# Kernel optimization log

Measured on AMD Instinct MI355X. Metric: run time of the kernel, lower is better.

The kernel has to match this reference:

```python
import jax, jax.numpy as jnp
import numpy as np

B, L = 128, 200
NUM_C, D, M = 10000, 128, 64


def setup_inputs() -> dict:
    key = jax.random.key(0)
    ks = jax.random.split(key, 16)
    n = lambda k, s, sc=0.05: jax.random.normal(k, s, dtype=jnp.float32) * sc
    return {
        "q": jax.random.randint(ks[0], (B, L), 0, NUM_C),
        "r": jax.random.randint(ks[1], (B, L), 0, 2),
        "k_emb": n(ks[2], (NUM_C, D)),
        "v_emb": n(ks[3], (2, D)),
        "Mk": n(ks[4], (M, D), 0.2),   # kaiming_normal_
        "Mv0": n(ks[5], (M, D), 0.2),  # kaiming_normal_
        "f_W": n(ks[6], (D, 2 * D)), "f_b": jnp.zeros((D,), jnp.float32),
        "e_W": n(ks[7], (D, D)), "e_b": jnp.zeros((D,), jnp.float32),
        "a_W": n(ks[8], (D, D)), "a_b": jnp.zeros((D,), jnp.float32),
        "ab_W": n(ks[9], (1, D)), "ab_b": jnp.zeros((1,), jnp.float32),
        "df_W": n(ks[10], (1, D)), "df_b": jnp.zeros((1,), jnp.float32),
    }


def reference(q, r, k_emb, v_emb, Mk, Mv0, f_W, f_b, e_W, e_b, a_W, a_b, ab_W, ab_b, df_W, df_b):
    # Embeddings
    k = k_emb[q]                # [B, L, D] question key embedding
    v = k + v_emb[r]            # [B, L, D] value embedding

    # Attention over memory slots, erase/add gates
    w = jax.nn.softmax(jnp.einsum('bld,md->blm', k, Mk), axis=-1)   # [B, L, M]
    e = jax.nn.sigmoid(jnp.einsum('bld,ed->ble', v, e_W) + e_b)      # erase [B, L, D]
    a = jnp.tanh(jnp.einsum('bld,ed->ble', v, a_W) + a_b)            # add   [B, L, D]

    Mvt0 = jnp.broadcast_to(Mv0[None], (q.shape[0], Mv0.shape[0], Mv0.shape[1]))  # [B, M, D]

    def step(Mvt, inp):
        wt, et, at = inp  # [B,M], [B,D], [B,D]
        # read uses memory BEFORE this timestep's write (Mv[:, :-1] in torch)
        read = jnp.einsum('bm,bmd->bd', wt, Mvt)
        we = wt[:, :, None]
        Mvt_new = Mvt * (1.0 - we * et[:, None, :]) + we * at[:, None, :]
        return Mvt_new, read

    _, reads = jax.lax.scan(
        step, Mvt0,
        (w.transpose(1, 0, 2), e.transpose(1, 0, 2), a.transpose(1, 0, 2)))
    reads = reads.transpose(1, 0, 2)  # [B, L, D]

    f = jnp.tanh(jnp.concatenate([reads, k], axis=-1) @ f_W.T + f_b)  # [B, L, D]
    stu_ability = jnp.tanh(f @ ab_W.T + ab_b)   # [B, L, 1] (dropout is identity in eval)
    que_diff = jnp.tanh(k @ df_W.T + df_b)      # [B, L, 1]
    p = jax.nn.sigmoid(3.0 * stu_ability - que_diff)
    return p.squeeze(-1)  # [B, L]
```

## Files before the change

kernel.cpp:

```cpp
#include <hip/hip_runtime.h>

typedef unsigned short ushort_t;
typedef _Float16 f16_t;
typedef short bf16x8 __attribute__((ext_vector_type(8)));
typedef float f32x4 __attribute__((ext_vector_type(4)));

#define B_ 128
#define L_ 200
#define D_ 128
#define M_ 64

__device__ __forceinline__ float fast_sigmoid(float x) {
    return 1.f / (1.f + __expf(-x));
}

__device__ __forceinline__ float fast_tanh(float x) {
    float xc = fminf(fmaxf(x, -15.f), 15.f);
    float e = __expf(2.f * xc);
    return (e - 1.f) / (e + 1.f);
}

__device__ __forceinline__ ushort_t f2bf(float f) {
    union { float f; unsigned int u; } x;
    x.f = f;
    unsigned int u = x.u;
    unsigned int r = (u + 0x7FFFu + ((u >> 16) & 1u)) >> 16;
    return (ushort_t)r;
}

__device__ __forceinline__ uint4 pack8(float4 a, float4 b) {
    uint4 u;
    u.x = (unsigned)f2bf(a.x) | ((unsigned)f2bf(a.y) << 16);
    u.y = (unsigned)f2bf(a.z) | ((unsigned)f2bf(a.w) << 16);
    u.z = (unsigned)f2bf(b.x) | ((unsigned)f2bf(b.y) << 16);
    u.w = (unsigned)f2bf(b.z) | ((unsigned)f2bf(b.w) << 16);
    return u;
}

__device__ __forceinline__ unsigned pack_ea(float e, float a) {
    union { f16_t h[2]; unsigned u; } p;
    p.h[0] = (f16_t)e;
    p.h[1] = (f16_t)a;
    return p.u;
}

__device__ __forceinline__ float2 unpack_ea(unsigned u) {
    union { unsigned u; f16_t h[2]; } p;
    p.u = u;
    float2 r;
    r.x = (float)p.h[0];
    r.y = (float)p.h[1];
    return r;
}

#define F_WQ   0u
#define F_EAQ  1638400u
#define F_FKQ  8192000u
#define F_RD   11468800u
#define F_DIFF 14745600u
#define F_PACK 14771200u
#define WPACK_N 57344
#define FPACK_N 16384

__global__ __launch_bounds__(256) void k_pack(
    const float* __restrict__ Mk, const float* __restrict__ eW,
    const float* __restrict__ aW, const float* __restrict__ fW,
    ushort_t* __restrict__ Wpack, ushort_t* __restrict__ Fpack)
{
    int i = blockIdx.x * 256 + threadIdx.x;
    if (i < WPACK_N) {
        int g = i >> 9, lane = (i >> 3) & 63, j = i & 7;
        int nt = g >> 2, ks = g & 3;
        int col = nt * 16 + (lane & 15);
        int d = ks * 32 + ((lane >> 4) << 3) + j;
        float v;
        if (col < 64)       v = Mk[col * 128 + d];
        else if (col < 192) v = eW[(col - 64) * 128 + d];
        else if (col < 320) v = aW[(col - 192) * 128 + d];
        else                v = fW[(col - 320) * 256 + 128 + d];
        Wpack[i] = f2bf(v);
    } else if (i < WPACK_N + FPACK_N) {
        int e = i - WPACK_N;
        int g = e >> 9, lane = (e >> 3) & 63, j = e & 7;
        int nt = g >> 2, ks = g & 3;
        int col = nt * 16 + (lane & 15);
        int d = ks * 32 + ((lane >> 4) << 3) + j;
        Fpack[e] = f2bf(fW[col * 256 + d]);
    }
}

__device__ __forceinline__ void loadB4(const ushort_t* __restrict__ base,
                                       int nt, int lane, bf16x8* b) {
    const ushort_t* p = base + (nt * 256 + lane) * 8;
    b[0] = *(const bf16x8*)(p);
    b[1] = *(const bf16x8*)(p + 512);
    b[2] = *(const bf16x8*)(p + 1024);
    b[3] = *(const bf16x8*)(p + 1536);
}

__global__ __launch_bounds__(512) void k_pre_mfma(
    const int* __restrict__ q, const int* __restrict__ r,
    const float* __restrict__ k_emb, const float* __restrict__ v_emb,
    const ushort_t* __restrict__ Wpack,
    const float* __restrict__ e_b, const float* __restrict__ a_b,
    const float* __restrict__ df_W, const float* __restrict__ df_b,
    float* __restrict__ wq, unsigned* __restrict__ eaq,
    f16_t* __restrict__ fkq, float* __restrict__ diffq)
{
    __shared__ ushort_t skA[8192];
    __shared__ ushort_t svA[8192];
    __shared__ float slog[64 * 68];

    const int tid = threadIdx.x;
    const int pos0 = blockIdx.x * 64;
    const int wave = tid >> 6;
    const int lane = tid & 63;
    const int mt = wave & 3;
    const int nh = wave >> 2;

    #pragma unroll
    for (int i = 0; i < 2; i++) {
        int E = tid + 512 * i;
        int mtile = E >> 8, ks = (E >> 6) & 3, le = E & 63;
        int prow = pos0 + mtile * 16 + (le & 15);
        int dof = ks * 32 + ((le >> 4) << 3);
        int qv = q[prow], rv = r[prow];
        const float4* kp = (const float4*)(k_emb + qv * 128 + dof);
        float4 ka = kp[0], kb = kp[1];
        const float4* vp = (const float4*)(v_emb + rv * 128 + dof);
        float4 va = vp[0], vb = vp[1];
        *(uint4*)&skA[E * 8] = pack8(ka, kb);
        float4 s0, s1;
        s0.x = ka.x + va.x; s0.y = ka.y + va.y; s0.z = ka.z + va.z; s0.w = ka.w + va.w;
        s1.x = kb.x + vb.x; s1.y = kb.y + vb.y; s1.z = kb.z + vb.z; s1.w = kb.w + vb.w;
        *(uint4*)&svA[E * 8] = pack8(s0, s1);
    }
    __syncthreads();

    bf16x8 A[4];
    {
        const ushort_t* src = nh ? svA : skA;
        #pragma unroll
        for (int ks = 0; ks < 4; ks++)
            A[ks] = *(const bf16x8*)&src[((mt * 4 + ks) * 64 + lane) * 8];
    }

    const int col = lane & 15;
    const int quad = lane >> 4;
    const int rbase = mt * 16 + quad * 4;

    if (nh == 0) {
        bf16x8 Bb[2][4];
        loadB4(Wpack, 0, lane, Bb[0]);
        #pragma unroll
        for (int j = 0; j < 12; j++) {
            if (j < 11) {
                int jn = j + 1;
                loadB4(Wpack, (jn < 4) ? jn : jn + 16, lane, Bb[jn & 1]);
            }
            f32x4 acc = {0.f, 0.f, 0.f, 0.f};
            #pragma unroll
            for (int ks = 0; ks < 4; ks++)
                acc = __builtin_amdgcn_mfma_f32_16x16x32_bf16(A[ks], Bb[j & 1][ks], acc, 0, 0, 0);
            if (j < 4) {
                #pragma unroll
                for (int reg = 0; reg < 4; reg++)
                    slog[(rbase + reg) * 68 + j * 16 + col] = acc[reg];
            } else {
                int c = (j - 4) * 16 + col;
                #pragma unroll
                for (int reg = 0; reg < 4; reg++)
                    fkq[(pos0 + rbase + reg) * 128 + c] = (f16_t)acc[reg];
            }
        }
        {
            int row = tid >> 2, ln = tid & 3;
            const float* lr = slog + row * 68 + ln * 16;
            float v[16];
            #pragma unroll
            for (int j = 0; j < 16; j++) v[j] = lr[j];
            float mx = v[0];
            #pragma unroll
            for (int j = 1; j < 16; j++) mx = fmaxf(mx, v[j]);
            mx = fmaxf(mx, __shfl_xor(mx, 1));
            mx = fmaxf(mx, __shfl_xor(mx, 2));
            float s = 0.f;
            #pragma unroll
            for (int j = 0; j < 16; j++) { v[j] = __expf(v[j] - mx); s += v[j]; }
            s += __shfl_xor(s, 1); s += __shfl_xor(s, 2);
            float inv = 1.f / s;
            float* wout = wq + (pos0 + row) * 64 + ln * 16;
            #pragma unroll
            for (int j4 = 0; j4 < 4; j4++) {
                float4 o;
                o.x = v[j4 * 4 + 0] * inv;
                o.y = v[j4 * 4 + 1] * inv;
                o.z = v[j4 * 4 + 2] * inv;
                o.w = v[j4 * 4 + 3] * inv;
                *(float4*)(wout + j4 * 4) = o;
            }
        }
    } else {
        bf16x8 Be[2][4], Ba[2][4];
        loadB4(Wpack, 4, lane, Be[0]);
        loadB4(Wpack, 12, lane, Ba[0]);
        #pragma unroll
        for (int i = 0; i < 8; i++) {
            if (i < 7) {
                loadB4(Wpack, 5 + i, lane, Be[(i + 1) & 1]);
                loadB4(Wpack, 13 + i, lane, Ba[(i + 1) & 1]);
            }
            f32x4 ae = {0.f, 0.f, 0.f, 0.f};
            f32x4 aa = {0.f, 0.f, 0.f, 0.f};
            #pragma unroll
            for (int ks = 0; ks < 4; ks++) {
                ae = __builtin_amdgcn_mfma_f32_16x16x32_bf16(A[ks], Be[i & 1][ks], ae, 0, 0, 0);
                aa = __builtin_amdgcn_mfma_f32_16x16x32_bf16(A[ks], Ba[i & 1][ks], aa, 0, 0, 0);
            }
            int c = i * 16 + col;
            float ebv = e_b[c], abv = a_b[c];
            #pragma unroll
            for (int reg = 0; reg < 4; reg++) {
                float ev = fast_sigmoid(ae[reg] + ebv);
                float av = fast_tanh(aa[reg] + abv);
                eaq[(pos0 + rbase + reg) * 128 + c] = pack_ea(ev, av);
            }
        }
        {
            int t2 = tid - 256;
            int row = t2 >> 2, ln = t2 & 3;
            int pos = pos0 + row;
            int qv = q[pos];
            const float4* kp = (const float4*)(k_emb + qv * 128) + ln * 8;
            const float4* dfp = (const float4*)df_W + ln * 8;
            float s = 0.f;
            #pragma unroll
            for (int j = 0; j < 8; j++) {
                float4 a = kp[j], b = dfp[j];
                s = fmaf(a.x, b.x, fmaf(a.y, b.y, fmaf(a.z, b.z, fmaf(a.w, b.w, s))));
            }
            s += __shfl_xor(s, 1); s += __shfl_xor(s, 2);
            if (ln == 0) diffq[pos] = fast_tanh(s + df_b[0]);
        }
    }
}

#define SC_PREFETCH(wX, eX, cN)                                            \
    _Pragma("unroll")                                                      \
    for (int tt = 0; tt < 8; tt++) {                                       \
        wX[2 * tt]     = wb4[((cN) * 8 + tt) * 16 + sc * 2];               \
        wX[2 * tt + 1] = wb4[((cN) * 8 + tt) * 16 + sc * 2 + 1];           \
        eX[tt]         = unpack_ea(eab[((cN) * 8 + tt) * 128]);            \
    }

#define SC_COMPUTE(wX, eX, bb)                                             \
    _Pragma("unroll")                                                      \
    for (int tt = 0; tt < 8; tt++) {                                       \
        float4 u = wX[2 * tt], v = wX[2 * tt + 1];                         \
        float2 ea = eX[tt];                                                \
        float ev = ea.x, av = ea.y, ne = -ev;                              \
        float r0 = u.x * Mv[0];                                            \
        float r1 = u.y * Mv[1];                                            \
        r0 = fmaf(u.z, Mv[2], r0); r1 = fmaf(u.w, Mv[3], r1);              \
        r0 = fmaf(v.x, Mv[4], r0); r1 = fmaf(v.y, Mv[5], r1);              \
        r0 = fmaf(v.z, Mv[6], r0); r1 = fmaf(v.w, Mv[7], r1);              \
        Mv[0] = fmaf(u.x, fmaf(ne, Mv[0], av), Mv[0]);                     \
        Mv[1] = fmaf(u.y, fmaf(ne, Mv[1], av), Mv[1]);                     \
        Mv[2] = fmaf(u.z, fmaf(ne, Mv[2], av), Mv[2]);                     \
        Mv[3] = fmaf(u.w, fmaf(ne, Mv[3], av), Mv[3]);                     \
        Mv[4] = fmaf(v.x, fmaf(ne, Mv[4], av), Mv[4]);                     \
        Mv[5] = fmaf(v.y, fmaf(ne, Mv[5], av), Mv[5]);                     \
        Mv[6] = fmaf(v.z, fmaf(ne, Mv[6], av), Mv[6]);                     \
        Mv[7] = fmaf(v.w, fmaf(ne, Mv[7], av), Mv[7]);                     \
        pbuf[bb][sc][tt][lane] = r0 + r1;                                  \
    }

#define SC_REDUCE(bb, c0) {                                                \
        float s = pbuf[bb][0][wv][lane] + pbuf[bb][1][wv][lane]            \
                + pbuf[bb][2][wv][lane] + pbuf[bb][3][wv][lane]            \
                + pbuf[bb][4][wv][lane] + pbuf[bb][5][wv][lane]            \
                + pbuf[bb][6][wv][lane] + pbuf[bb][7][wv][lane];           \
        rbase[((c0) * 8 + wv) * 128 + lane] = f2bf(s);                     \
    }

__global__ __launch_bounds__(512, 2) void k_scan(
    const float* __restrict__ wq, const unsigned* __restrict__ eaq,
    const float* __restrict__ Mv0, ushort_t* __restrict__ reads)
{
    __shared__ float pbuf[2][8][8][64];

    const int tid = threadIdx.x;
    const int b = blockIdx.x >> 1;
    const int dh = blockIdx.x & 1;
    const int wv = tid >> 6;
    const int sc = __builtin_amdgcn_readfirstlane(wv);
    const int lane = tid & 63;
    const int d = dh * 64 + lane;

    float Mv[8];
    #pragma unroll
    for (int j = 0; j < 8; j++) Mv[j] = Mv0[(sc * 8 + j) * D_ + d];

    const float4* wb4 = (const float4*)(wq + b * (L_ * M_));
    const unsigned* eab = eaq + b * (L_ * 128) + d;
    ushort_t* rbase = reads + b * (L_ * D_) + dh * 64;

    float4 wA[16], wB[16];
    float2 eA[8], eB[8];

    SC_PREFETCH(wA, eA, 0);

    for (int cc = 0; cc < 12; cc++) {
        const int c0 = 2 * cc;
        SC_PREFETCH(wB, eB, c0 + 1);
        SC_COMPUTE(wA, eA, 0);
        __syncthreads();
        SC_REDUCE(0, c0);
        SC_PREFETCH(wA, eA, c0 + 2);
        SC_COMPUTE(wB, eB, 1);
        __syncthreads();
        SC_REDUCE(1, c0 + 1);
    }
    SC_COMPUTE(wA, eA, 0);
    __syncthreads();
    SC_REDUCE(0, 24);
}

__global__ __launch_bounds__(512) void k_final_mfma(
    const ushort_t* __restrict__ reads, const f16_t* __restrict__ fkq,
    const float* __restrict__ diffq, const ushort_t* __restrict__ Fpack,
    const float* __restrict__ f_b, const float* __restrict__ ab_W,
    const float* __restrict__ ab_b, float* __restrict__ out)
{
    __shared__ ushort_t srA[8192];
    __shared__ float sab[64 * 2];

    const int tid = threadIdx.x;
    const int pos0 = blockIdx.x * 64;
    const int wave = tid >> 6;
    const int lane = tid & 63;
    const int mt = wave & 3;
    const int half = wave >> 2;

    #pragma unroll
    for (int i = 0; i < 2; i++) {
        int E = tid + 512 * i;
        int mtile = E >> 8, ks = (E >> 6) & 3, le = E & 63;
        int prow = pos0 + mtile * 16 + (le & 15);
        int dof = ks * 32 + ((le >> 4) << 3);
        *(uint4*)&srA[E * 8] = *(const uint4*)(reads + prow * 128 + dof);
    }

    const int col = lane & 15;
    const int quad = lane >> 4;
    const int rbase = mt * 16 + quad * 4;

    float fkv[16];
    #pragma unroll
    for (int i = 0; i < 4; i++)
        #pragma unroll
        for (int reg = 0; reg < 4; reg++)
            fkv[i * 4 + reg] = (float)fkq[(pos0 + rbase + reg) * 128 + (half * 4 + i) * 16 + col];

    __syncthreads();

    bf16x8 A[4];
    #pragma unroll
    for (int ks = 0; ks < 4; ks++)
        A[ks] = *(const bf16x8*)&srA[((mt * 4 + ks) * 64 + lane) * 8];

    float abacc[4] = {0.f, 0.f, 0.f, 0.f};

    bf16x8 Bb[2][4];
    loadB4(Fpack, half * 4, lane, Bb[0]);
    #pragma unroll
    for (int i = 0; i < 4; i++) {
        if (i < 3) loadB4(Fpack, half * 4 + i + 1, lane, Bb[(i + 1) & 1]);
        f32x4 acc = {0.f, 0.f, 0.f, 0.f};
        #pragma unroll
        for (int ks = 0; ks < 4; ks++)
            acc = __builtin_amdgcn_mfma_f32_16x16x32_bf16(A[ks], Bb[i & 1][ks], acc, 0, 0, 0);
        int c = (half * 4 + i) * 16 + col;
        float fb = f_b[c];
        float abw = ab_W[c];
        #pragma unroll
        for (int reg = 0; reg < 4; reg++) {
            float fv = fast_tanh(acc[reg] + fkv[i * 4 + reg] + fb);
            abacc[reg] = fmaf(abw, fv, abacc[reg]);
        }
    }

    #pragma unroll
    for (int reg = 0; reg < 4; reg++) {
        float v = abacc[reg];
        v += __shfl_xor(v, 1); v += __shfl_xor(v, 2);
        v += __shfl_xor(v, 4); v += __shfl_xor(v, 8);
        abacc[reg] = v;
    }
    if (col == 0) {
        #pragma unroll
        for (int reg = 0; reg < 4; reg++)
            sab[(rbase + reg) * 2 + half] = abacc[reg];
    }
    __syncthreads();
    if (tid < 64) {
        float ab = fast_tanh(sab[tid * 2] + sab[tid * 2 + 1] + ab_b[0]);
        int pos = pos0 + tid;
        out[pos] = fast_sigmoid(3.f * ab - diffq[pos]);
    }
}

extern "C" void kernel_launch(void* const* d_in, const int* in_sizes, int n_in,
                              void* d_out, int out_size, void* d_ws, size_t ws_size,
                              hipStream_t stream)
{
    const int*   q     = (const int*)d_in[0];
    const int*   r     = (const int*)d_in[1];
    const float* k_emb = (const float*)d_in[2];
    const float* v_emb = (const float*)d_in[3];
    const float* Mk    = (const float*)d_in[4];
    const float* Mv0   = (const float*)d_in[5];
    const float* f_W   = (const float*)d_in[6];
    const float* f_b   = (const float*)d_in[7];
    const float* e_W   = (const float*)d_in[8];
    const float* e_b   = (const float*)d_in[9];
    const float* a_W   = (const float*)d_in[10];
    const float* a_b   = (const float*)d_in[11];
    const float* ab_W  = (const float*)d_in[12];
    const float* ab_b  = (const float*)d_in[13];
    const float* df_W  = (const float*)d_in[14];
    const float* df_b  = (const float*)d_in[15];

    float* ws = (float*)d_ws;
    float* out = (float*)d_out;
    unsigned* eaq_u   = (unsigned*)(ws + F_EAQ);
    f16_t*    fkq_h   = (f16_t*)(ws + F_FKQ);
    ushort_t* reads_b = (ushort_t*)(ws + F_RD);
    ushort_t* Wpack = (ushort_t*)(ws + F_PACK);
    ushort_t* Fpack = Wpack + WPACK_N;

    k_pack<<<288, 256, 0, stream>>>(Mk, e_W, a_W, f_W, Wpack, Fpack);

    k_pre_mfma<<<400, 512, 0, stream>>>(
        q, r, k_emb, v_emb, Wpack, e_b, a_b, df_W, df_b,
        ws + F_WQ, eaq_u, fkq_h, ws + F_DIFF);

    k_scan<<<256, 512, 0, stream>>>(
        ws + F_WQ, eaq_u, Mv0, reads_b);

    k_final_mfma<<<400, 512, 0, stream>>>(
        reads_b, fkq_h, ws + F_DIFF, Fpack,
        f_b, ab_W, ab_b, out);
}
```

Before: 146.3 us.

## Fuse four kernels into one cooperative kernel with grid-wide syncs

Merges the weight-pack, pre-MFMA projection, recurrent scan and final MFMA kernels into a single cooperative launch of 256 blocks, separated by grid.sync barriers. Each block loops over the 400 position tiles in the pre and final phases. The aim is to remove launch overheads and inter-kernel gaps. In exchange, the pre and final phases run as 256 blocks over 400 tiles, which is uneven, and each grid barrier has its own cost.

```diff
diff --git a/kernel.cpp b/kernel.cpp
--- a/kernel.cpp
+++ b/kernel.cpp
@@ -1,4 +1,7 @@
 #include <hip/hip_runtime.h>
+#include <hip/hip_cooperative_groups.h>
+
+namespace cg = cooperative_groups;
 
 typedef unsigned short ushort_t;
 typedef _Float16 f16_t;
@@ -62,32 +65,32 @@
 #define WPACK_N 57344
 #define FPACK_N 16384
 
-__global__ __launch_bounds__(256) void k_pack(
-    const float* __restrict__ Mk, const float* __restrict__ eW,
-    const float* __restrict__ aW, const float* __restrict__ fW,
-    ushort_t* __restrict__ Wpack, ushort_t* __restrict__ Fpack)
-{
-    int i = blockIdx.x * 256 + threadIdx.x;
-    if (i < WPACK_N) {
-        int g = i >> 9, lane = (i >> 3) & 63, j = i & 7;
-        int nt = g >> 2, ks = g & 3;
-        int col = nt * 16 + (lane & 15);
-        int d = ks * 32 + ((lane >> 4) << 3) + j;
-        float v;
-        if (col < 64)       v = Mk[col * 128 + d];
-        else if (col < 192) v = eW[(col - 64) * 128 + d];
-        else if (col < 320) v = aW[(col - 192) * 128 + d];
-        else                v = fW[(col - 320) * 256 + 128 + d];
-        Wpack[i] = f2bf(v);
-    } else if (i < WPACK_N + FPACK_N) {
-        int e = i - WPACK_N;
-        int g = e >> 9, lane = (e >> 3) & 63, j = e & 7;
-        int nt = g >> 2, ks = g & 3;
-        int col = nt * 16 + (lane & 15);
-        int d = ks * 32 + ((lane >> 4) << 3) + j;
-        Fpack[e] = f2bf(fW[col * 256 + d]);
-    }
-}
+struct KParams {
+    const int* q;
+    const int* r;
+    const float* k_emb;
+    const float* v_emb;
+    const float* Mk;
+    const float* Mv0;
+    const float* f_W;
+    const float* f_b;
+    const float* e_W;
+    const float* e_b;
+    const float* a_W;
+    const float* a_b;
+    const float* ab_W;
+    const float* ab_b;
+    const float* df_W;
+    const float* df_b;
+    float* wq;
+    unsigned* eaq;
+    f16_t* fkq;
+    float* diffq;
+    ushort_t* reads;
+    ushort_t* Wpack;
+    ushort_t* Fpack;
+    float* out;
+};
 
 __device__ __forceinline__ void loadB4(const ushort_t* __restrict__ base,
                                        int nt, int lane, bf16x8* b) {
@@ -98,152 +101,7 @@
     b[3] = *(const bf16x8*)(p + 1536);
 }
 
-__global__ __launch_bounds__(512) void k_pre_mfma(
-    const int* __restrict__ q, const int* __restrict__ r,
-    const float* __restrict__ k_emb, const float* __restrict__ v_emb,
-    const ushort_t* __restrict__ Wpack,
-    const float* __restrict__ e_b, const float* __restrict__ a_b,
-    const float* __restrict__ df_W, const float* __restrict__ df_b,
-    float* __restrict__ wq, unsigned* __restrict__ eaq,
-    f16_t* __restrict__ fkq, float* __restrict__ diffq)
-{
-    __shared__ ushort_t skA[8192];
-    __shared__ ushort_t svA[8192];
-    __shared__ float slog[64 * 68];
-
-    const int tid = threadIdx.x;
-    const int pos0 = blockIdx.x * 64;
-    const int wave = tid >> 6;
-    const int lane = tid & 63;
-    const int mt = wave & 3;
-    const int nh = wave >> 2;
-
-    #pragma unroll
-    for (int i = 0; i < 2; i++) {
-        int E = tid + 512 * i;
-        int mtile = E >> 8, ks = (E >> 6) & 3, le = E & 63;
-        int prow = pos0 + mtile * 16 + (le & 15);
-        int dof = ks * 32 + ((le >> 4) << 3);
-        int qv = q[prow], rv = r[prow];
-        const float4* kp = (const float4*)(k_emb + qv * 128 + dof);
-        float4 ka = kp[0], kb = kp[1];
-        const float4* vp = (const float4*)(v_emb + rv * 128 + dof);
-        float4 va = vp[0], vb = vp[1];
-        *(uint4*)&skA[E * 8] = pack8(ka, kb);
-        float4 s0, s1;
-        s0.x = ka.x + va.x; s0.y = ka.y + va.y; s0.z = ka.z + va.z; s0.w = ka.w + va.w;
-        s1.x = kb.x + vb.x; s1.y = kb.y + vb.y; s1.z = kb.z + vb.z; s1.w = kb.w + vb.w;
-        *(uint4*)&svA[E * 8] = pack8(s0, s1);
-    }
-    __syncthreads();
-
-    bf16x8 A[4];
-    {
-        const ushort_t* src = nh ? svA : skA;
-        #pragma unroll
-        for (int ks = 0; ks < 4; ks++)
-            A[ks] = *(const bf16x8*)&src[((mt * 4 + ks) * 64 + lane) * 8];
-    }
-
-    const int col = lane & 15;
-    const int quad = lane >> 4;
-    const int rbase = mt * 16 + quad * 4;
-
-    if (nh == 0) {
-        bf16x8 Bb[2][4];
-        loadB4(Wpack, 0, lane, Bb[0]);
-        #pragma unroll
-        for (int j = 0; j < 12; j++) {
-            if (j < 11) {
-                int jn = j + 1;
-                loadB4(Wpack, (jn < 4) ? jn : jn + 16, lane, Bb[jn & 1]);
-            }
-            f32x4 acc = {0.f, 0.f, 0.f, 0.f};
-            #pragma unroll
-            for (int ks = 0; ks < 4; ks++)
-                acc = __builtin_amdgcn_mfma_f32_16x16x32_bf16(A[ks], Bb[j & 1][ks], acc, 0, 0, 0);
-            if (j < 4) {
-                #pragma unroll
-                for (int reg = 0; reg < 4; reg++)
-                    slog[(rbase + reg) * 68 + j * 16 + col] = acc[reg];
-            } else {
-                int c = (j - 4) * 16 + col;
-                #pragma unroll
-                for (int reg = 0; reg < 4; reg++)
-                    fkq[(pos0 + rbase + reg) * 128 + c] = (f16_t)acc[reg];
-            }
-        }
-        {
-            int row = tid >> 2, ln = tid & 3;
-            const float* lr = slog + row * 68 + ln * 16;
-            float v[16];
-            #pragma unroll
-            for (int j = 0; j < 16; j++) v[j] = lr[j];
-            float mx = v[0];
-            #pragma unroll
-            for (int j = 1; j < 16; j++) mx = fmaxf(mx, v[j]);
-            mx = fmaxf(mx, __shfl_xor(mx, 1));
-            mx = fmaxf(mx, __shfl_xor(mx, 2));
-            float s = 0.f;
-            #pragma unroll
-            for (int j = 0; j < 16; j++) { v[j] = __expf(v[j] - mx); s += v[j]; }
-            s += __shfl_xor(s, 1); s += __shfl_xor(s, 2);
-            float inv = 1.f / s;
-            float* wout = wq + (pos0 + row) * 64 + ln * 16;
-            #pragma unroll
-            for (int j4 = 0; j4 < 4; j4++) {
-                float4 o;
-                o.x = v[j4 * 4 + 0] * inv;
-                o.y = v[j4 * 4 + 1] * inv;
-                o.z = v[j4 * 4 + 2] * inv;
-                o.w = v[j4 * 4 + 3] * inv;
-                *(float4*)(wout + j4 * 4) = o;
-            }
-        }
-    } else {
-        bf16x8 Be[2][4], Ba[2][4];
-        loadB4(Wpack, 4, lane, Be[0]);
-        loadB4(Wpack, 12, lane, Ba[0]);
-        #pragma unroll
-        for (int i = 0; i < 8; i++) {
-            if (i < 7) {
-                loadB4(Wpack, 5 + i, lane, Be[(i + 1) & 1]);
-                loadB4(Wpack, 13 + i, lane, Ba[(i + 1) & 1]);
-            }
-            f32x4 ae = {0.f, 0.f, 0.f, 0.f};
-            f32x4 aa = {0.f, 0.f, 0.f, 0.f};
-            #pragma unroll
-            for (int ks = 0; ks < 4; ks++) {
-                ae = __builtin_amdgcn_mfma_f32_16x16x32_bf16(A[ks], Be[i & 1][ks], ae, 0, 0, 0);
-                aa = __builtin_amdgcn_mfma_f32_16x16x32_bf16(A[ks], Ba[i & 1][ks], aa, 0, 0, 0);
-            }
-            int c = i * 16 + col;
-            float ebv = e_b[c], abv = a_b[c];
-            #pragma unroll
-            for (int reg = 0; reg < 4; reg++) {
-                float ev = fast_sigmoid(ae[reg] + ebv);
-                float av = fast_tanh(aa[reg] + abv);
-                eaq[(pos0 + rbase + reg) * 128 + c] = pack_ea(ev, av);
-            }
-        }
-        {
-            int t2 = tid - 256;
-            int row = t2 >> 2, ln = t2 & 3;
-            int pos = pos0 + row;
-            int qv = q[pos];
-            const float4* kp = (const float4*)(k_emb + qv * 128) + ln * 8;
-            const float4* dfp = (const float4*)df_W + ln * 8;
-            float s = 0.f;
-            #pragma unroll
-            for (int j = 0; j < 8; j++) {
-                float4 a = kp[j], b = dfp[j];
-                s = fmaf(a.x, b.x, fmaf(a.y, b.y, fmaf(a.z, b.z, fmaf(a.w, b.w, s))));
-            }
-            s += __shfl_xor(s, 1); s += __shfl_xor(s, 2);
-            if (ln == 0) diffq[pos] = fast_tanh(s + df_b[0]);
-        }
-    }
-}
+#define PBUF(bb, w, t, l) (((bb) * 4096) + ((w) * 512) + ((t) * 64) + (l))
 
 #define SC_PREFETCH(wX, eX, cN)                                            \
     _Pragma("unroll")                                                      \
@@ -272,141 +130,345 @@
         Mv[5] = fmaf(v.y, fmaf(ne, Mv[5], av), Mv[5]);                     \
         Mv[6] = fmaf(v.z, fmaf(ne, Mv[6], av), Mv[6]);                     \
         Mv[7] = fmaf(v.w, fmaf(ne, Mv[7], av), Mv[7]);                     \
-        pbuf[bb][sc][tt][lane] = r0 + r1;                                  \
+        pbuf[PBUF(bb, sc, tt, lane)] = r0 + r1;                            \
     }
 
 #define SC_REDUCE(bb, c0) {                                                \
-        float s = pbuf[bb][0][wv][lane] + pbuf[bb][1][wv][lane]            \
-                + pbuf[bb][2][wv][lane] + pbuf[bb][3][wv][lane]            \
-                + pbuf[bb][4][wv][lane] + pbuf[bb][5][wv][lane]            \
-                + pbuf[bb][6][wv][lane] + pbuf[bb][7][wv][lane];           \
+        float s = pbuf[PBUF(bb, 0, wv, lane)] + pbuf[PBUF(bb, 1, wv, lane)]\
+                + pbuf[PBUF(bb, 2, wv, lane)] + pbuf[PBUF(bb, 3, wv, lane)]\
+                + pbuf[PBUF(bb, 4, wv, lane)] + pbuf[PBUF(bb, 5, wv, lane)]\
+                + pbuf[PBUF(bb, 6, wv, lane)] + pbuf[PBUF(bb, 7, wv, lane)];\
         rbase[((c0) * 8 + wv) * 128 + lane] = f2bf(s);                     \
     }
 
-__global__ __launch_bounds__(512, 2) void k_scan(
-    const float* __restrict__ wq, const unsigned* __restrict__ eaq,
-    const float* __restrict__ Mv0, ushort_t* __restrict__ reads)
+__global__ __launch_bounds__(512, 2) void k_fused(KParams P)
 {
-    __shared__ float pbuf[2][8][8][64];
+    __shared__ __align__(16) char smem[50688];
 
     const int tid = threadIdx.x;
-    const int b = blockIdx.x >> 1;
-    const int dh = blockIdx.x & 1;
-    const int wv = tid >> 6;
-    const int sc = __builtin_amdgcn_readfirstlane(wv);
+    const int bid = blockIdx.x;
+    const int wave = tid >> 6;
     const int lane = tid & 63;
-    const int d = dh * 64 + lane;
-
-    float Mv[8];
-    #pragma unroll
-    for (int j = 0; j < 8; j++) Mv[j] = Mv0[(sc * 8 + j) * D_ + d];
-
-    const float4* wb4 = (const float4*)(wq + b * (L_ * M_));
-    const unsigned* eab = eaq + b * (L_ * 128) + d;
-    ushort_t* rbase = reads + b * (L_ * D_) + dh * 64;
-
-    float4 wA[16], wB[16];
-    float2 eA[8], eB[8];
-
-    SC_PREFETCH(wA, eA, 0);
-
-    for (int cc = 0; cc < 12; cc++) {
-        const int c0 = 2 * cc;
-        SC_PREFETCH(wB, eB, c0 + 1);
+
+    cg::grid_group grid = cg::this_grid();
+
+    {
+        const float* __restrict__ Mk = P.Mk;
+        const float* __restrict__ eW = P.e_W;
+        const float* __restrict__ aW = P.a_W;
+        const float* __restrict__ fW = P.f_W;
+        int i = bid * 512 + tid;
+        if (i < WPACK_N) {
+            int g = i >> 9, ln = (i >> 3) & 63, j = i & 7;
+            int nt = g >> 2, ks = g & 3;
+            int col = nt * 16 + (ln & 15);
+            int d = ks * 32 + ((ln >> 4) << 3) + j;
+            float v;
+            if (col < 64)       v = Mk[col * 128 + d];
+            else if (col < 192) v = eW[(col - 64) * 128 + d];
+            else if (col < 320) v = aW[(col - 192) * 128 + d];
+            else                v = fW[(col - 320) * 256 + 128 + d];
+            P.Wpack[i] = f2bf(v);
+        } else if (i < WPACK_N + FPACK_N) {
+            int e = i - WPACK_N;
+            int g = e >> 9, ln = (e >> 3) & 63, j = e & 7;
+            int nt = g >> 2, ks = g & 3;
+            int col = nt * 16 + (ln & 15);
+            int d = ks * 32 + ((ln >> 4) << 3) + j;
+            P.Fpack[e] = f2bf(fW[col * 256 + d]);
+        }
+    }
+    __threadfence();
+    grid.sync();
+
+    {
+        ushort_t* skA = (ushort_t*)smem;
+        ushort_t* svA = skA + 8192;
+        float* slog = (float*)(smem + 32768);
+
+        const int* __restrict__ q = P.q;
+        const int* __restrict__ r = P.r;
+        const float* __restrict__ k_emb = P.k_emb;
+        const float* __restrict__ v_emb = P.v_emb;
+        const ushort_t* __restrict__ Wpack = P.Wpack;
+        const float* __restrict__ e_b = P.e_b;
+        const float* __restrict__ a_b = P.a_b;
+        const float* __restrict__ df_W = P.df_W;
+        const float* __restrict__ df_b = P.df_b;
+        float* __restrict__ wq = P.wq;
+        unsigned* __restrict__ eaq = P.eaq;
+        f16_t* __restrict__ fkq = P.fkq;
+        float* __restrict__ diffq = P.diffq;
+
+        const int mt = wave & 3;
+        const int nh = wave >> 2;
+
+        for (int t = bid; t < 400; t += 256) {
+            const int pos0 = t * 64;
+
+            #pragma unroll
+            for (int i = 0; i < 2; i++) {
+                int E = tid + 512 * i;
+                int mtile = E >> 8, ks = (E >> 6) & 3, le = E & 63;
+                int prow = pos0 + mtile * 16 + (le & 15);
+                int dof = ks * 32 + ((le >> 4) << 3);
+                int qv = q[prow], rv = r[prow];
+                const float4* kp = (const float4*)(k_emb + qv * 128 + dof);
+                float4 ka = kp[0], kb = kp[1];
+                const float4* vp = (const float4*)(v_emb + rv * 128 + dof);
+                float4 va = vp[0], vb = vp[1];
+                *(uint4*)&skA[E * 8] = pack8(ka, kb);
+                float4 s0, s1;
+                s0.x = ka.x + va.x; s0.y = ka.y + va.y; s0.z = ka.z + va.z; s0.w = ka.w + va.w;
+                s1.x = kb.x + vb.x; s1.y = kb.y + vb.y; s1.z = kb.z + vb.z; s1.w = kb.w + vb.w;
+                *(uint4*)&svA[E * 8] = pack8(s0, s1);
+            }
+            __syncthreads();
+
+            bf16x8 A[4];
+            {
+                const ushort_t* src = nh ? svA : skA;
+                #pragma unroll
+                for (int ks = 0; ks < 4; ks++)
+                    A[ks] = *(const bf16x8*)&src[((mt * 4 + ks) * 64 + lane) * 8];
+            }
+
+            const int col = lane & 15;
+            const int quad = lane >> 4;
+            const int rbase = mt * 16 + quad * 4;
+
+            if (nh == 0) {
+                bf16x8 Bb[2][4];
+                loadB4(Wpack, 0, lane, Bb[0]);
+                #pragma unroll
+                for (int j = 0; j < 12; j++) {
+                    if (j < 11) {
+                        int jn = j + 1;
+                        loadB4(Wpack, (jn < 4) ? jn : jn + 16, lane, Bb[jn & 1]);
+                    }
+                    f32x4 acc = {0.f, 0.f, 0.f, 0.f};
+                    #pragma unroll
+                    for (int ks = 0; ks < 4; ks++)
+                        acc = __builtin_amdgcn_mfma_f32_16x16x32_bf16(A[ks], Bb[j & 1][ks], acc, 0, 0, 0);
+                    if (j < 4) {
+                        #pragma unroll
+                        for (int reg = 0; reg < 4; reg++)
+                            slog[(rbase + reg) * 68 + j * 16 + col] = acc[reg];
+                    } else {
+                        int c = (j - 4) * 16 + col;
+                        #pragma unroll
+                        for (int reg = 0; reg < 4; reg++)
+                            fkq[(pos0 + rbase + reg) * 128 + c] = (f16_t)acc[reg];
+                    }
+                }
+                {
+                    int row = tid >> 2, ln = tid & 3;
+                    const float* lr = slog + row * 68 + ln * 16;
+                    float v[16];
+                    #pragma unroll
+                    for (int j = 0; j < 16; j++) v[j] = lr[j];
+                    float mx = v[0];
+                    #pragma unroll
+                    for (int j = 1; j < 16; j++) mx = fmaxf(mx, v[j]);
+                    mx = fmaxf(mx, __shfl_xor(mx, 1));
+                    mx = fmaxf(mx, __shfl_xor(mx, 2));
+                    float s = 0.f;
+                    #pragma unroll
+                    for (int j = 0; j < 16; j++) { v[j] = __expf(v[j] - mx); s += v[j]; }
+                    s += __shfl_xor(s, 1); s += __shfl_xor(s, 2);
+                    float inv = 1.f / s;
+                    float* wout = wq + (pos0 + row) * 64 + ln * 16;
+                    #pragma unroll
+                    for (int j4 = 0; j4 < 4; j4++) {
+                        float4 o;
+                        o.x = v[j4 * 4 + 0] * inv;
+                        o.y = v[j4 * 4 + 1] * inv;
+                        o.z = v[j4 * 4 + 2] * inv;
+                        o.w = v[j4 * 4 + 3] * inv;
+                        *(float4*)(wout + j4 * 4) = o;
+                    }
+                }
+            } else {
+                bf16x8 Be[2][4], Ba[2][4];
+                loadB4(Wpack, 4, lane, Be[0]);
+                loadB4(Wpack, 12, lane, Ba[0]);
+                #pragma unroll
+                for (int i = 0; i < 8; i++) {
+                    if (i < 7) {
+                        loadB4(Wpack, 5 + i, lane, Be[(i + 1) & 1]);
+                        loadB4(Wpack, 13 + i, lane, Ba[(i + 1) & 1]);
+                    }
+                    f32x4 ae = {0.f, 0.f, 0.f, 0.f};
+                    f32x4 aa = {0.f, 0.f, 0.f, 0.f};
+                    #pragma unroll
+                    for (int ks = 0; ks < 4; ks++) {
+                        ae = __builtin_amdgcn_mfma_f32_16x16x32_bf16(A[ks], Be[i & 1][ks], ae, 0, 0, 0);
+                        aa = __builtin_amdgcn_mfma_f32_16x16x32_bf16(A[ks], Ba[i & 1][ks], aa, 0, 0, 0);
+                    }
+                    int c = i * 16 + col;
+                    float ebv = e_b[c], abv = a_b[c];
+                    #pragma unroll
+                    for (int reg = 0; reg < 4; reg++) {
+                        float ev = fast_sigmoid(ae[reg] + ebv);
+                        float av = fast_tanh(aa[reg] + abv);
+                        eaq[(pos0 + rbase + reg) * 128 + c] = pack_ea(ev, av);
+                    }
+                }
+                {
+                    int t2 = tid - 256;
+                    int row = t2 >> 2, ln = t2 & 3;
+                    int pos = pos0 + row;
+                    int qv = q[pos];
+                    const float4* kp = (const float4*)(k_emb + qv * 128) + ln * 8;
+                    const float4* dfp = (const float4*)df_W + ln * 8;
+                    float s = 0.f;
+                    #pragma unroll
+                    for (int j = 0; j < 8; j++) {
+                        float4 a = kp[j], b = dfp[j];
+                        s = fmaf(a.x, b.x, fmaf(a.y, b.y, fmaf(a.z, b.z, fmaf(a.w, b.w, s))));
+                    }
+                    s += __shfl_xor(s, 1); s += __shfl_xor(s, 2);
+                    if (ln == 0) diffq[pos] = fast_tanh(s + df_b[0]);
+                }
+            }
+            __syncthreads();
+        }
+    }
+    __threadfence();
+    grid.sync();
+
+    {
+        float* pbuf = (float*)smem;
+
+        const float* __restrict__ wq = P.wq;
+        const unsigned* __restrict__ eaq = P.eaq;
+        const float* __restrict__ Mv0 = P.Mv0;
+        ushort_t* __restrict__ reads = P.reads;
+
+        const int b = bid >> 1;
+        const int dh = bid & 1;
+        const int wv = wave;
+        const int sc = __builtin_amdgcn_readfirstlane(wv);
+        const int d = dh * 64 + lane;
+
+        float Mv[8];
+        #pragma unroll
+        for (int j = 0; j < 8; j++) Mv[j] = Mv0[(sc * 8 + j) * D_ + d];
+
+        const float4* wb4 = (const float4*)(wq + b * (L_ * M_));
+        const unsigned* eab = eaq + b * (L_ * 128) + d;
+        ushort_t* rbase = reads + b * (L_ * D_) + dh * 64;
+
+        float4 wA[16], wB[16];
+        float2 eA[8], eB[8];
+
+        SC_PREFETCH(wA, eA, 0);
+
+        for (int cc = 0; cc < 12; cc++) {
+            const int c0 = 2 * cc;
+            SC_PREFETCH(wB, eB, c0 + 1);
+            SC_COMPUTE(wA, eA, 0);
+            __syncthreads();
+            SC_REDUCE(0, c0);
+            SC_PREFETCH(wA, eA, c0 + 2);
+            SC_COMPUTE(wB, eB, 1);
+            __syncthreads();
+            SC_REDUCE(1, c0 + 1);
+        }
         SC_COMPUTE(wA, eA, 0);
         __syncthreads();
-        SC_REDUCE(0, c0);
-        SC_PREFETCH(wA, eA, c0 + 2);
-        SC_COMPUTE(wB, eB, 1);
-        __syncthreads();
-        SC_REDUCE(1, c0 + 1);
-    }
-    SC_COMPUTE(wA, eA, 0);
-    __syncthreads();
-    SC_REDUCE(0, 24);
-}
-
-__global__ __launch_bounds__(512) void k_final_mfma(
-    const ushort_t* __restrict__ reads, const f16_t* __restrict__ fkq,
-    const float* __restrict__ diffq, const ushort_t* __restrict__ Fpack,
-    const float* __restrict__ f_b, const float* __restrict__ ab_W,
-    const float* __restrict__ ab_b, float* __restrict__ out)
-{
-    __shared__ ushort_t srA[8192];
-    __shared__ float sab[64 * 2];
-
-    const int tid = threadIdx.x;
-    const int pos0 = blockIdx.x * 64;
-    const int wave = tid >> 6;
-    const int lane = tid & 63;
-    const int mt = wave & 3;
-    const int half = wave >> 2;
-
-    #pragma unroll
-    for (int i = 0; i < 2; i++) {
-        int E = tid + 512 * i;
-        int mtile = E >> 8, ks = (E >> 6) & 3, le = E & 63;
-        int prow = pos0 + mtile * 16 + (le & 15);
-        int dof = ks * 32 + ((le >> 4) << 3);
-        *(uint4*)&srA[E * 8] = *(const uint4*)(reads + prow * 128 + dof);
-    }
-
-    const int col = lane & 15;
-    const int quad = lane >> 4;
-    const int rbase = mt * 16 + quad * 4;
-
-    float fkv[16];
-    #pragma unroll
-    for (int i = 0; i < 4; i++)
-        #pragma unroll
-        for (int reg = 0; reg < 4; reg++)
-            fkv[i * 4 + reg] = (float)fkq[(pos0 + rbase + reg) * 128 + (half * 4 + i) * 16 + col];
-
-    __syncthreads();
-
-    bf16x8 A[4];
-    #pragma unroll
-    for (int ks = 0; ks < 4; ks++)
-        A[ks] = *(const bf16x8*)&srA[((mt * 4 + ks) * 64 + lane) * 8];
-
-    float abacc[4] = {0.f, 0.f, 0.f, 0.f};
-
-    bf16x8 Bb[2][4];
-    loadB4(Fpack, half * 4, lane, Bb[0]);
-    #pragma unroll
-    for (int i = 0; i < 4; i++) {
-        if (i < 3) loadB4(Fpack, half * 4 + i + 1, lane, Bb[(i + 1) & 1]);
-        f32x4 acc = {0.f, 0.f, 0.f, 0.f};
-        #pragma unroll
-        for (int ks = 0; ks < 4; ks++)
-            acc = __builtin_amdgcn_mfma_f32_16x16x32_bf16(A[ks], Bb[i & 1][ks], acc, 0, 0, 0);
-        int c = (half * 4 + i) * 16 + col;
-        float fb = f_b[c];
-        float abw = ab_W[c];
-        #pragma unroll
-        for (int reg = 0; reg < 4; reg++) {
-            float fv = fast_tanh(acc[reg] + fkv[i * 4 + reg] + fb);
-            abacc[reg] = fmaf(abw, fv, abacc[reg]);
+        SC_REDUCE(0, 24);
+    }
+    __threadfence();
+    grid.sync();
+
+    {
+        ushort_t* srA = (ushort_t*)smem;
+        float* sab = (float*)(smem + 16384);
+
+        const ushort_t* __restrict__ reads = P.reads;
+        const f16_t* __restrict__ fkq = P.fkq;
+        const float* __restrict__ diffq = P.diffq;
+        const ushort_t* __restrict__ Fpack = P.Fpack;
+        const float* __restrict__ f_b = P.f_b;
+        const float* __restrict__ ab_W = P.ab_W;
+        const float* __restrict__ ab_b = P.ab_b;
+        float* __restrict__ out = P.out;
+
+        const int mt = wave & 3;
+        const int half = wave >> 2;
+
+        for (int t = bid; t < 400; t += 256) {
+            const int pos0 = t * 64;
+
+            #pragma unroll
+            for (int i = 0; i < 2; i++) {
+                int E = tid + 512 * i;
+                int mtile = E >> 8, ks = (E >> 6) & 3, le = E & 63;
+                int prow = pos0 + mtile * 16 + (le & 15);
+                int dof = ks * 32 + ((le >> 4) << 3);
+                *(uint4*)&srA[E * 8] = *(const uint4*)(reads + prow * 128 + dof);
+            }
+
+            const int col = lane & 15;
+            const int quad = lane >> 4;
+            const int rbase = mt * 16 + quad * 4;
+
+            float fkv[16];
+            #pragma unroll
+            for (int i = 0; i < 4; i++)
+                #pragma unroll
+                for (int reg = 0; reg < 4; reg++)
+                    fkv[i * 4 + reg] = (float)fkq[(pos0 + rbase + reg) * 128 + (half * 4 + i) * 16 + col];
+
+            __syncthreads();
+
+            bf16x8 A[4];
+            #pragma unroll
+            for (int ks = 0; ks < 4; ks++)
+                A[ks] = *(const bf16x8*)&srA[((mt * 4 + ks) * 64 + lane) * 8];
+
+            float abacc[4] = {0.f, 0.f, 0.f, 0.f};
+
+            bf16x8 Bb[2][4];
+            loadB4(Fpack, half * 4, lane, Bb[0]);
+            #pragma unroll
+            for (int i = 0; i < 4; i++) {
+                if (i < 3) loadB4(Fpack, half * 4 + i + 1, lane, Bb[(i + 1) & 1]);
+                f32x4 acc = {0.f, 0.f, 0.f, 0.f};
+                #pragma unroll
+                for (int ks = 0; ks < 4; ks++)
+                    acc = __builtin_amdgcn_mfma_f32_16x16x32_bf16(A[ks], Bb[i & 1][ks], acc, 0, 0, 0);
+                int c = (half * 4 + i) * 16 + col;
+                float fb = f_b[c];
+                float abw = ab_W[c];
+                #pragma unroll
+                for (int reg = 0; reg < 4; reg++) {
+                    float fv = fast_tanh(acc[reg] + fkv[i * 4 + reg] + fb);
+                    abacc[reg] = fmaf(abw, fv, abacc[reg]);
+                }
+            }
+
+            #pragma unroll
+            for (int reg = 0; reg < 4; reg++) {
+                float v = abacc[reg];
+                v += __shfl_xor(v, 1); v += __shfl_xor(v, 2);
+                v += __shfl_xor(v, 4); v += __shfl_xor(v, 8);
+                abacc[reg] = v;
+            }
+            if (col == 0) {
+                #pragma unroll
+                for (int reg = 0; reg < 4; reg++)
+                    sab[(rbase + reg) * 2 + half] = abacc[reg];
+            }
+            __syncthreads();
+            if (tid < 64) {
+                float ab = fast_tanh(sab[tid * 2] + sab[tid * 2 + 1] + ab_b[0]);
+                int pos = pos0 + tid;
+                out[pos] = fast_sigmoid(3.f * ab - diffq[pos]);
+            }
+            __syncthreads();
         }
-    }
-
-    #pragma unroll
-    for (int reg = 0; reg < 4; reg++) {
-        float v = abacc[reg];
-        v += __shfl_xor(v, 1); v += __shfl_xor(v, 2);
-        v += __shfl_xor(v, 4); v += __shfl_xor(v, 8);
-        abacc[reg] = v;
-    }
-    if (col == 0) {
-        #pragma unroll
-        for (int reg = 0; reg < 4; reg++)
-            sab[(rbase + reg) * 2 + half] = abacc[reg];
-    }
-    __syncthreads();
-    if (tid < 64) {
-        float ab = fast_tanh(sab[tid * 2] + sab[tid * 2 + 1] + ab_b[0]);
-        int pos = pos0 + tid;
-        out[pos] = fast_sigmoid(3.f * ab - diffq[pos]);
     }
 }
 
@@ -414,41 +476,36 @@
                               void* d_out, int out_size, void* d_ws, size_t ws_size,
                               hipStream_t stream)
 {
-    const int*   q     = (const int*)d_in[0];
-    const int*   r     = (const int*)d_in[1];
-    const float* k_emb = (const float*)d_in[2];
-    const float* v_emb = (const float*)d_in[3];
-    const float* Mk    = (const float*)d_in[4];
-    const float* Mv0   = (const float*)d_in[5];
-    const float* f_W   = (const float*)d_in[6];
-    const float* f_b   = (const float*)d_in[7];
-    const float* e_W   = (const float*)d_in[8];
-    const float* e_b   = (const float*)d_in[9];
-    const float* a_W   = (const float*)d_in[10];
-    const float* a_b   = (const float*)d_in[11];
-    const float* ab_W  = (const float*)d_in[12];
-    const float* ab_b  = (const float*)d_in[13];
-    const float* df_W  = (const float*)d_in[14];
-    const float* df_b  = (const float*)d_in[15];
-
     float* ws = (float*)d_ws;
-    float* out = (float*)d_out;
-    unsigned* eaq_u   = (unsigned*)(ws + F_EAQ);
-    f16_t*    fkq_h   = (f16_t*)(ws + F_FKQ);
-    ushort_t* reads_b = (ushort_t*)(ws + F_RD);
     ushort_t* Wpack = (ushort_t*)(ws + F_PACK);
-    ushort_t* Fpack = Wpack + WPACK_N;
-
-    k_pack<<<288, 256, 0, stream>>>(Mk, e_W, a_W, f_W, Wpack, Fpack);
-
-    k_pre_mfma<<<400, 512, 0, stream>>>(
-        q, r, k_emb, v_emb, Wpack, e_b, a_b, df_W, df_b,
-        ws + F_WQ, eaq_u, fkq_h, ws + F_DIFF);
-
-    k_scan<<<256, 512, 0, stream>>>(
-        ws + F_WQ, eaq_u, Mv0, reads_b);
-
-    k_final_mfma<<<400, 512, 0, stream>>>(
-        reads_b, fkq_h, ws + F_DIFF, Fpack,
-        f_b, ab_W, ab_b, out);
-}
+
+    KParams P;
+    P.q     = (const int*)d_in[0];
+    P.r     = (const int*)d_in[1];
+    P.k_emb = (const float*)d_in[2];
+    P.v_emb = (const float*)d_in[3];
+    P.Mk    = (const float*)d_in[4];
+    P.Mv0   = (const float*)d_in[5];
+    P.f_W   = (const float*)d_in[6];
+    P.f_b   = (const float*)d_in[7];
+    P.e_W   = (const float*)d_in[8];
+    P.e_b   = (const float*)d_in[9];
+    P.a_W   = (const float*)d_in[10];
+    P.a_b   = (const float*)d_in[11];
+    P.ab_W  = (const float*)d_in[12];
+    P.ab_b  = (const float*)d_in[13];
+    P.df_W  = (const float*)d_in[14];
+    P.df_b  = (const float*)d_in[15];
+    P.wq    = ws + F_WQ;
+    P.eaq   = (unsigned*)(ws + F_EAQ);
+    P.fkq   = (f16_t*)(ws + F_FKQ);
+    P.diffq = ws + F_DIFF;
+    P.reads = (ushort_t*)(ws + F_RD);
+    P.Wpack = Wpack;
+    P.Fpack = Wpack + WPACK_N;
+    P.out   = (float*)d_out;
+
+    void* args[] = { &P };
+    hipLaunchCooperativeKernel((const void*)k_fused, dim3(256), dim3(512),
+                               args, 0, stream);
+}
```

Measured after the change: 409.6 us. 180% more time.
